# Performance work log

Measured on AMD Instinct MI355X. Metric: run time of the kernel, lower is better.

The kernel has to match this reference:

```python
import jax, jax.numpy as jnp
import numpy as np

N = 50000      # nodes
E = 800000     # edges (before self-loops)
DIN = 128
DH = 16        # per-head channels, layer 1
H = 8          # heads, layer 1
DOUT = 128     # layer 2 output (heads=1)
EDIM = 8       # edge_attr dim (unused by math: edge_dim=None in GATConv)
EPS_BN = 1e-5
NEG_SLOPE = 0.2


def _gat_conv(x, edge_index, W, a_src, a_dst, bias, heads, ch):
    """PyG GATConv (concat=True, add_self_loops=True, edge_dim=None)."""
    n = x.shape[0]
    loop = jnp.arange(n, dtype=edge_index.dtype)
    src = jnp.concatenate([edge_index[0], loop])  # [E+N]
    dst = jnp.concatenate([edge_index[1], loop])
    h = (x @ W).reshape(n, heads, ch)             # [N,H,C]
    s_src = jnp.einsum('nhc,hc->nh', h, a_src)    # [N,H]
    s_dst = jnp.einsum('nhc,hc->nh', h, a_dst)
    e = jax.nn.leaky_relu(s_src[src] + s_dst[dst], NEG_SLOPE)  # [E+N,H]
    # segment softmax over incoming edges of each dst node
    m = jax.ops.segment_max(e, dst, num_segments=n)
    ex = jnp.exp(e - m[dst])
    den = jax.ops.segment_sum(ex, dst, num_segments=n)
    alpha = ex / (den[dst] + 1e-16)               # [E+N,H]
    out = jax.ops.segment_sum(alpha[:, :, None] * h[src], dst, num_segments=n)
    return out.reshape(n, heads * ch) + bias


def _bn_selu(x, gamma, beta):
    # BatchNorm1d in training mode (batch statistics, biased variance) + SELU.
    mu = x.mean(axis=0)
    var = x.var(axis=0)
    xn = (x - mu) * jax.lax.rsqrt(var + EPS_BN)
    return jax.nn.selu(gamma * xn + beta)


def setup_inputs() -> dict:
    key = jax.random.key(0)
    ks = jax.random.split(key, 12)
    x = jax.random.normal(ks[0], (N, DIN), jnp.float32)
    edge_index = jax.random.randint(ks[1], (2, E), 0, N, jnp.int32)
    edge_attr = jax.random.normal(ks[2], (E, EDIM), jnp.float32)
    W1 = jax.random.normal(ks[3], (DIN, H * DH), jnp.float32) / np.sqrt(DIN)
    a_src1 = jax.random.normal(ks[4], (H, DH), jnp.float32) / np.sqrt(DH)
    a_dst1 = jax.random.normal(ks[5], (H, DH), jnp.float32) / np.sqrt(DH)
    b1 = jnp.zeros((H * DH,), jnp.float32)
    g1 = jnp.ones((H * DH,), jnp.float32)
    beta1 = jnp.zeros((H * DH,), jnp.float32)
    W2 = jax.random.normal(ks[6], (H * DH, DOUT), jnp.float32) / np.sqrt(H * DH)
    a_src2 = jax.random.normal(ks[7], (1, DOUT), jnp.float32) / np.sqrt(DOUT)
    a_dst2 = jax.random.normal(ks[8], (1, DOUT), jnp.float32) / np.sqrt(DOUT)
    b2 = jnp.zeros((DOUT,), jnp.float32)
    g2 = jnp.ones((DOUT,), jnp.float32)
    beta2 = jnp.zeros((DOUT,), jnp.float32)
    return dict(x=x, edge_index=edge_index, edge_attr=edge_attr,
                W1=W1, a_src1=a_src1, a_dst1=a_dst1, b1=b1, g1=g1, beta1=beta1,
                W2=W2, a_src2=a_src2, a_dst2=a_dst2, b2=b2, g2=g2, beta2=beta2)


def reference(x, edge_index, edge_attr,
              W1, a_src1, a_dst1, b1, g1, beta1,
              W2, a_src2, a_dst2, b2, g2, beta2):
    # edge_attr is unused: GATConv built with edge_dim=None ignores edge features.
    h = _gat_conv(x, edge_index, W1, a_src1, a_dst1, b1, H, DH)   # [N, H*DH]
    h = _bn_selu(h, g1, beta1)                                    # dropout = identity (eval)
    h = _gat_conv(h, edge_index, W2, a_src2, a_dst2, b2, 1, DOUT) # [N, DOUT]
    h = _bn_selu(h, g2, beta2)
    return h
```

## Files before the change

### kernel.cpp

```cpp
#include <hip/hip_runtime.h>

#define SELU_SCALE 1.0507009873554805f
#define SELU_ALPHA 1.6732632423543772f

typedef __attribute__((ext_vector_type(8))) short short8;
typedef __attribute__((ext_vector_type(4))) float f32x4;

#define BCAP 10240

static __device__ __forceinline__ float leaky02(float v) {
  return v > 0.0f ? v : 0.2f * v;
}

static __device__ __forceinline__ ushort f2bf(float f) {
  uint b = __float_as_uint(f);
  return (ushort)((b + 0x7fffu + ((b >> 16) & 1u)) >> 16);
}
static __device__ __forceinline__ float bf2f(ushort u) {
  return __uint_as_float(((uint)u) << 16);
}

static __device__ __forceinline__ float selu_f(float y) {
  return y > 0.f ? SELU_SCALE * y : SELU_SCALE * SELU_ALPHA * (__expf(y) - 1.f);
}

static __device__ __forceinline__ void load8(const float* p, float* xv, bool ok) {
  float4 xa = make_float4(0.f, 0.f, 0.f, 0.f), xb = xa;
  if (ok) {
    xa = *(const float4*)p;
    xb = *(const float4*)(p + 4);
  }
  xv[0] = xa.x; xv[1] = xa.y; xv[2] = xa.z; xv[3] = xa.w;
  xv[4] = xb.x; xv[5] = xb.y; xv[6] = xb.z; xv[7] = xb.w;
}
static __device__ __forceinline__ void load8(const ushort* p, float* xv, bool ok) {
  ushort4 ua = make_ushort4(0, 0, 0, 0), ub = ua;
  if (ok) {
    ua = *(const ushort4*)p;
    ub = *(const ushort4*)(p + 4);
  }
  xv[0] = bf2f(ua.x); xv[1] = bf2f(ua.y); xv[2] = bf2f(ua.z); xv[3] = bf2f(ua.w);
  xv[4] = bf2f(ub.x); xv[5] = bf2f(ub.y); xv[6] = bf2f(ub.z); xv[7] = bf2f(ub.w);
}

__global__ __launch_bounds__(256) void pack_kernel(const float* __restrict__ W1,
                                                   const float* __restrict__ W2,
                                                   ushort* __restrict__ Wp1,
                                                   ushort* __restrict__ Wp2,
                                                   float* __restrict__ zbase, int zwords) {
  if (blockIdx.x == 128) {
    for (int i = threadIdx.x; i < zwords; i += 256) zbase[i] = 0.f;
    return;
  }
  int idx = blockIdx.x * 256 + threadIdx.x;
  const float* W = (idx < 16384) ? W1 : W2;
  ushort* Wp = (idx < 16384) ? Wp1 : Wp2;
  int t = idx & 16383;
  int b = t & 7, i = (t >> 3) & 15, g = (t >> 7) & 3, kt = (t >> 9) & 3, ct = t >> 11;
  int k = kt * 32 + g * 8 + b, col = ct * 16 + i;
  Wp[t] = f2bf(W[k * 128 + col]);
}

template <int HEADS, bool BN, typename XT>
static __device__ __forceinline__ void gemm_body(
    int blk, const XT* __restrict__ X, const ushort* __restrict__ Wp,
    ushort* __restrict__ H, const float* __restrict__ asr, const float* __restrict__ adt,
    float* __restrict__ ssrc, float* __restrict__ sdst, int n,
    const float* __restrict__ stats, const float* __restrict__ gamma,
    const float* __restrict__ beta) {
  __shared__ float sc[128], sh[128];
  if (BN) {
    int t = threadIdx.x;
    if (t < 128) {
      float invN = 1.0f / (float)n;
      float mu = stats[t] * invN;
      float var = stats[128 + t] * invN - mu * mu;
      float rs = rsqrtf(var + 1e-5f);
      float s = gamma[t] * rs;
      sc[t] = s;
      sh[t] = beta[t] - s * mu;
    }
    __syncthreads();
  }
  const int tid = threadIdx.x;
  const int w = tid >> 6, l = tid & 63;
  const int lj = l & 15, lg = l >> 4;
  const int row = blk * 64 + w * 16 + lj;
  const bool rowok = row < n;
  const XT* xrow = X + (size_t)row * 128;

  f32x4 acc[8];
#pragma unroll
  for (int ct = 0; ct < 8; ++ct) acc[ct] = (f32x4){0.f, 0.f, 0.f, 0.f};

#pragma unroll
  for (int kt = 0; kt < 4; ++kt) {
    const int k0 = kt * 32 + lg * 8;
    float xv[8];
    load8(xrow + k0, xv, rowok);
    if (BN) {
#pragma unroll
      for (int b = 0; b < 8; ++b) xv[b] = selu_f(xv[b] * sc[k0 + b] + sh[k0 + b]);
    }
    short8 bx;
#pragma unroll
    for (int b = 0; b < 8; ++b) bx[b] = (short)f2bf(xv[b]);
#pragma unroll
    for (int ct = 0; ct < 8; ++ct) {
      short8 af = *(const short8*)(Wp + ((((ct * 4 + kt) * 4 + lg) * 16 + lj) << 3));
      acc[ct] = __builtin_amdgcn_mfma_f32_16x16x32_bf16(af, bx, acc[ct], 0, 0, 0);
    }
  }

  if (rowok) {
#pragma unroll
    for (int ct = 0; ct < 8; ++ct) {
      ushort4 h4;
      h4.x = f2bf(acc[ct][0]);
      h4.y = f2bf(acc[ct][1]);
      h4.z = f2bf(acc[ct][2]);
      h4.w = f2bf(acc[ct][3]);
      *(ushort4*)&H[(size_t)row * 128 + ct * 16 + lg * 4] = h4;
    }
  }

  if (HEADS == 8) {
    float ps[8], pd[8];
#pragma unroll
    for (int ct = 0; ct < 8; ++ct) {
      float4 av = *(const float4*)&asr[ct * 16 + lg * 4];
      float4 dv = *(const float4*)&adt[ct * 16 + lg * 4];
      ps[ct] = acc[ct][0] * av.x + acc[ct][1] * av.y + acc[ct][2] * av.z + acc[ct][3] * av.w;
      pd[ct] = acc[ct][0] * dv.x + acc[ct][1] * dv.y + acc[ct][2] * dv.z + acc[ct][3] * dv.w;
      ps[ct] += __shfl_xor(ps[ct], 16);
      ps[ct] += __shfl_xor(ps[ct], 32);
      pd[ct] += __shfl_xor(pd[ct], 16);
      pd[ct] += __shfl_xor(pd[ct], 32);
    }
    if (lg == 0 && rowok) {
      *(float4*)&ssrc[(size_t)row * 8] = make_float4(ps[0], ps[1], ps[2], ps[3]);
      *(float4*)&ssrc[(size_t)row * 8 + 4] = make_float4(ps[4], ps[5], ps[6], ps[7]);
      *(float4*)&sdst[(size_t)row * 8] = make_float4(pd[0], pd[1], pd[2], pd[3]);
      *(float4*)&sdst[(size_t)row * 8 + 4] = make_float4(pd[4], pd[5], pd[6], pd[7]);
    }
  } else {
    float ps = 0.f, pd = 0.f;
#pragma unroll
    for (int ct = 0; ct < 8; ++ct) {
      float4 av = *(const float4*)&asr[ct * 16 + lg * 4];
      float4 dv = *(const float4*)&adt[ct * 16 + lg * 4];
      ps += acc[ct][0] * av.x + acc[ct][1] * av.y + acc[ct][2] * av.z + acc[ct][3] * av.w;
      pd += acc[ct][0] * dv.x + acc[ct][1] * dv.y + acc[ct][2] * dv.z + acc[ct][3] * dv.w;
    }
    ps += __shfl_xor(ps, 16);
    ps += __shfl_xor(ps, 32);
    pd += __shfl_xor(pd, 16);
    pd += __shfl_xor(pd, 32);
    if (lg == 0 && rowok) {
      ssrc[row] = ps;
      sdst[row] = pd;
    }
  }
}

__global__ __launch_bounds__(256) void gemm1_bucket_kernel(
    const float* __restrict__ X, const ushort* __restrict__ Wp, ushort* __restrict__ H,
    const float* __restrict__ asr, const float* __restrict__ adt,
    float* __restrict__ ssrc, float* __restrict__ sdst, int n,
    const int* __restrict__ ei, int* __restrict__ gcur, uint* __restrict__ bucket,
    int nE, int EA, int NB, int gb) {
  if (blockIdx.x < gb) {
    gemm_body<8, false, float>(blockIdx.x, X, Wp, H, asr, adt, ssrc, sdst, n,
                               nullptr, nullptr, nullptr);
    return;
  }
  __shared__ int lcnt[128];
  __shared__ int lbase[128];
  int tid = threadIdx.x;
  if (tid < 128) lcnt[tid] = 0;
  __syncthreads();
  int e0 = (blockIdx.x - gb) * 1024;
  uint ent[4];
  int bk[4], lp[4];
#pragma unroll
  for (int j = 0; j < 4; ++j) {
    int e = e0 + j * 256 + tid;
    bk[j] = -1;
    if (e < EA) {
      int src, dst;
      if (e < nE) {
        src = ei[e];
        dst = ei[nE + e];
      } else {
        src = dst = e - nE;
      }
      bk[j] = dst >> 9;
      ent[j] = ((uint)src << 9) | (uint)(dst & 511);
      lp[j] = atomicAdd(&lcnt[bk[j]], 1);
    }
  }
  __syncthreads();
  if (tid < NB && lcnt[tid] > 0) lbase[tid] = atomicAdd(&gcur[tid], lcnt[tid]);
  __syncthreads();
#pragma unroll
  for (int j = 0; j < 4; ++j) {
    if (bk[j] >= 0) bucket[(size_t)bk[j] * BCAP + lbase[bk[j]] + lp[j]] = ent[j];
  }
}

__global__ __launch_bounds__(256) void gemm2_kernel(
    const ushort* __restrict__ X, const ushort* __restrict__ Wp, ushort* __restrict__ H,
    const float* __restrict__ asr, const float* __restrict__ adt,
    float* __restrict__ ssrc, float* __restrict__ sdst, int n,
    const float* __restrict__ stats, const float* __restrict__ gamma,
    const float* __restrict__ beta) {
  gemm_body<1, true, ushort>(blockIdx.x, X, Wp, H, asr, adt, ssrc, sdst, n,
                             stats, gamma, beta);
}

__global__ __launch_bounds__(1024) void csrbuild_kernel(const int* __restrict__ gcur,
                                                        const uint* __restrict__ bucket,
                                                        int* __restrict__ offs,
                                                        int* __restrict__ csr,
                                                        int n, int NB) {
  __shared__ int ldeg[512];
  __shared__ int loff[512];
  __shared__ int lwsum[8];
  __shared__ int partial[2];
  int b = blockIdx.x, tid = threadIdx.x;
  int lane = tid & 63, w = tid >> 6;
  if (tid < 128) {
    int v = (tid < b) ? gcur[tid] : 0;
#pragma unroll
    for (int s = 1; s < 64; s <<= 1) v += __shfl_xor(v, s);
    if (lane == 0) partial[tid >> 6] = v;
  }
  if (tid < 512) ldeg[tid] = 0;
  __syncthreads();
  int base = partial[0] + partial[1];
  int cnt = gcur[b];
  const uint* bb = bucket + (size_t)b * BCAP;
  for (int k = tid; k < cnt; k += 1024) atomicAdd(&ldeg[bb[k] & 511], 1);
  __syncthreads();
  int v = 0, x = 0;
  if (tid < 512) {
    v = ldeg[tid];
    x = v;
#pragma unroll
    for (int s = 1; s < 64; s <<= 1) {
      int t = __shfl_up(x, s);
      if (lane >= s) x += t;
    }
    if (lane == 63) lwsum[w] = x;
  }
  __syncthreads();
  if (w == 0 && lane < 8) {
    int wv = lwsum[lane];
    int y = wv;
#pragma unroll
    for (int s = 1; s < 8; s <<= 1) {
      int t = __shfl_up(y, s);
      if (lane >= s) y += t;
    }
    lwsum[lane] = y - wv;
  }
  __syncthreads();
  if (tid < 512) {
    int excl = x - v + lwsum[w];
    loff[tid] = excl;
    int node = b * 512 + tid;
    if (node < n) offs[node] = base + excl;
  }
  if (b == NB - 1 && tid == 0) offs[n] = base + cnt;
  __syncthreads();
  if (tid < 512) ldeg[tid] = loff[tid];
  __syncthreads();
  for (int k = tid; k < cnt; k += 1024) {
    uint e = bb[k];
    int pos = atomicAdd(&ldeg[e & 511], 1);
    csr[base + pos] = (int)(e >> 9);
  }
}

__global__ __launch_bounds__(256) void agg1_kernel(const ushort* __restrict__ h1,
                                                   const int* __restrict__ csr,
                                                   const int* __restrict__ offs,
                                                   const float* __restrict__ ssrc,
                                                   const float* __restrict__ sdst,
                                                   const float* __restrict__ bias,
                                                   ushort* __restrict__ outb, int nN) {
  int wid = (blockIdx.x * blockDim.x + threadIdx.x) >> 6;
  int lane = threadIdx.x & 63;
  int half = lane >> 5, ll = lane & 31;
  if (wid >= nN) return;
  int c = ll * 4;
  int h = ll >> 2;
  float sd = sdst[wid * 8 + h];
  int beg = offs[wid];
  int deg = offs[wid + 1] - beg;
  float a0 = 0.f, a1 = 0.f, a2 = 0.f, a3 = 0.f, den = 0.f;
  int i = half;
  for (; i + 6 < deg; i += 8) {
    int s0 = csr[beg + i];
    int s1 = csr[beg + i + 2];
    int s2 = csr[beg + i + 4];
    int s3 = csr[beg + i + 6];
    float e0 = ssrc[s0 * 8 + h];
    float e1 = ssrc[s1 * 8 + h];
    float e2 = ssrc[s2 * 8 + h];
    float e3 = ssrc[s3 * 8 + h];
    ushort4 u0 = *(const ushort4*)&h1[(size_t)s0 * 128 + c];
    ushort4 u1 = *(const ushort4*)&h1[(size_t)s1 * 128 + c];
    ushort4 u2 = *(const ushort4*)&h1[(size_t)s2 * 128 + c];
    ushort4 u3 = *(const ushort4*)&h1[(size_t)s3 * 128 + c];
    float A0 = __expf(leaky02(e0 + sd));
    float A1 = __expf(leaky02(e1 + sd));
    float A2 = __expf(leaky02(e2 + sd));
    float A3 = __expf(leaky02(e3 + sd));
    a0 += A0 * bf2f(u0.x) + A1 * bf2f(u1.x) + A2 * bf2f(u2.x) + A3 * bf2f(u3.x);
    a1 += A0 * bf2f(u0.y) + A1 * bf2f(u1.y) + A2 * bf2f(u2.y) + A3 * bf2f(u3.y);
    a2 += A0 * bf2f(u0.z) + A1 * bf2f(u1.z) + A2 * bf2f(u2.z) + A3 * bf2f(u3.z);
    a3 += A0 * bf2f(u0.w) + A1 * bf2f(u1.w) + A2 * bf2f(u2.w) + A3 * bf2f(u3.w);
    den += (A0 + A1) + (A2 + A3);
  }
  for (; i < deg; i += 2) {
    int s0 = csr[beg + i];
    float e0 = ssrc[s0 * 8 + h];
    ushort4 u0 = *(const ushort4*)&h1[(size_t)s0 * 128 + c];
    float A0 = __expf(leaky02(e0 + sd));
    a0 += A0 * bf2f(u0.x);
    a1 += A0 * bf2f(u0.y);
    a2 += A0 * bf2f(u0.z);
    a3 += A0 * bf2f(u0.w);
    den += A0;
  }
  a0 += __shfl_xor(a0, 32);
  a1 += __shfl_xor(a1, 32);
  a2 += __shfl_xor(a2, 32);
  a3 += __shfl_xor(a3, 32);
  den += __shfl_xor(den, 32);
  if (half == 0) {
    float invd = 1.0f / (den + 1e-16f);
    float4 bv = *(const float4*)&bias[c];
    ushort4 o;
    o.x = f2bf(a0 * invd + bv.x);
    o.y = f2bf(a1 * invd + bv.y);
    o.z = f2bf(a2 * invd + bv.z);
    o.w = f2bf(a3 * invd + bv.w);
    *(ushort4*)&outb[(size_t)wid * 128 + c] = o;
  }
}

__global__ __launch_bounds__(256) void agg2_kernel(const ushort* __restrict__ h2,
                                                   const int* __restrict__ csr,
                                                   const int* __restrict__ offs,
                                                   const float* __restrict__ ssrc,
                                                   const float* __restrict__ sdst,
                                                   const float* __restrict__ bias,
                                                   float* __restrict__ out, int nN) {
  int wid = (blockIdx.x * blockDim.x + threadIdx.x) >> 6;
  int lane = threadIdx.x & 63;
  int half = lane >> 5, ll = lane & 31;
  if (wid >= nN) return;
  int c = ll * 4;
  float sd = sdst[wid];
  int beg = offs[wid];
  int deg = offs[wid + 1] - beg;
  float a0 = 0.f, a1 = 0.f, a2 = 0.f, a3 = 0.f, den = 0.f;
  int i = half;
  for (; i + 6 < deg; i += 8) {
    int s0 = csr[beg + i];
    int s1 = csr[beg + i + 2];
    int s2 = csr[beg + i + 4];
    int s3 = csr[beg + i + 6];
    float e0 = ssrc[s0];
    float e1 = ssrc[s1];
    float e2 = ssrc[s2];
    float e3 = ssrc[s3];
    ushort4 u0 = *(const ushort4*)&h2[(size_t)s0 * 128 + c];
    ushort4 u1 = *(const ushort4*)&h2[(size_t)s1 * 128 + c];
    ushort4 u2 = *(const ushort4*)&h2[(size_t)s2 * 128 + c];
    ushort4 u3 = *(const ushort4*)&h2[(size_t)s3 * 128 + c];
    float A0 = __expf(leaky02(e0 + sd));
    float A1 = __expf(leaky02(e1 + sd));
    float A2 = __expf(leaky02(e2 + sd));
    float A3 = __expf(leaky02(e3 + sd));
    a0 += A0 * bf2f(u0.x) + A1 * bf2f(u1.x) + A2 * bf2f(u2.x) + A3 * bf2f(u3.x);
    a1 += A0 * bf2f(u0.y) + A1 * bf2f(u1.y) + A2 * bf2f(u2.y) + A3 * bf2f(u3.y);
    a2 += A0 * bf2f(u0.z) + A1 * bf2f(u1.z) + A2 * bf2f(u2.z) + A3 * bf2f(u3.z);
    a3 += A0 * bf2f(u0.w) + A1 * bf2f(u1.w) + A2 * bf2f(u2.w) + A3 * bf2f(u3.w);
    den += (A0 + A1) + (A2 + A3);
  }
  for (; i < deg; i += 2) {
    int s0 = csr[beg + i];
    float e0 = ssrc[s0];
    ushort4 u0 = *(const ushort4*)&h2[(size_t)s0 * 128 + c];
    float A0 = __expf(leaky02(e0 + sd));
    a0 += A0 * bf2f(u0.x);
    a1 += A0 * bf2f(u0.y);
    a2 += A0 * bf2f(u0.z);
    a3 += A0 * bf2f(u0.w);
    den += A0;
  }
  a0 += __shfl_xor(a0, 32);
  a1 += __shfl_xor(a1, 32);
  a2 += __shfl_xor(a2, 32);
  a3 += __shfl_xor(a3, 32);
  den += __shfl_xor(den, 32);
  if (half == 0) {
    float invd = 1.0f / (den + 1e-16f);
    float4 bv = *(const float4*)&bias[c];
    *(float4*)&out[(size_t)wid * 128 + c] =
        make_float4(a0 * invd + bv.x, a1 * invd + bv.y, a2 * invd + bv.z, a3 * invd + bv.w);
  }
}

__global__ __launch_bounds__(256) void stats_bf16_kernel(const ushort* __restrict__ X,
                                                         float* __restrict__ stats, int n) {
  __shared__ float red[256];
  int tid = threadIdx.x;
  int c = tid & 127;
  int half = tid >> 7;
  float s = 0.f, sq = 0.f;
  int rbeg = (int)blockIdx.x * 64 + half;
  int rend = min((int)(blockIdx.x + 1) * 64, n);
#pragma unroll 4
  for (int r = rbeg; r < rend; r += 2) {
    float v = bf2f(X[(size_t)r * 128 + c]);
    s += v;
    sq += v * v;
  }
  red[tid] = s;
  __syncthreads();
  float s2 = (half == 0) ? s + red[tid + 128] : 0.f;
  __syncthreads();
  red[tid] = sq;
  __syncthreads();
  if (half == 0) {
    float sq2 = sq + red[tid + 128];
    atomicAdd(&stats[c], s2);
    atomicAdd(&stats[128 + c], sq2);
  }
}

__global__ __launch_bounds__(256) void stats_kernel(const float* __restrict__ X,
                                                    float* __restrict__ stats, int n) {
  __shared__ float red[256];
  int tid = threadIdx.x;
  int c = tid & 127;
  int half = tid >> 7;
  float s = 0.f, sq = 0.f;
  int rbeg = (int)blockIdx.x * 64 + half;
  int rend = min((int)(blockIdx.x + 1) * 64, n);
#pragma unroll 4
  for (int r = rbeg; r < rend; r += 2) {
    float v = X[(size_t)r * 128 + c];
    s += v;
    sq += v * v;
  }
  red[tid] = s;
  __syncthreads();
  float s2 = (half == 0) ? s + red[tid + 128] : 0.f;
  __syncthreads();
  red[tid] = sq;
  __syncthreads();
  if (half == 0) {
    float sq2 = sq + red[tid + 128];
    atomicAdd(&stats[c], s2);
    atomicAdd(&stats[128 + c], sq2);
  }
}

__global__ __launch_bounds__(256) void bnselu_kernel(const float* __restrict__ X,
                                                     const float* __restrict__ stats,
                                                     const float* __restrict__ gamma,
                                                     const float* __restrict__ beta,
                                                     float* __restrict__ Y, int n) {
  int gid = blockIdx.x * blockDim.x + threadIdx.x;
  if (gid >= n * 32) return;
  int c = (gid & 31) * 4;
  int r = gid >> 5;
  float invN = 1.0f / (float)n;
  float4 x = *(const float4*)&X[(size_t)r * 128 + c];
  float o[4];
#pragma unroll
  for (int j = 0; j < 4; ++j) {
    float xx = (j == 0) ? x.x : (j == 1) ? x.y : (j == 2) ? x.z : x.w;
    float mu = stats[c + j] * invN;
    float var = stats[128 + c + j] * invN - mu * mu;
    float rs = rsqrtf(var + 1e-5f);
    float y = gamma[c + j] * ((xx - mu) * rs) + beta[c + j];
    o[j] = selu_f(y);
  }
  *(float4*)&Y[(size_t)r * 128 + c] = make_float4(o[0], o[1], o[2], o[3]);
}

extern "C" void kernel_launch(void* const* d_in, const int* in_sizes, int n_in,
                              void* d_out, int out_size, void* d_ws, size_t ws_size,
                              hipStream_t stream) {
  const float* x   = (const float*)d_in[0];
  const int*   ei  = (const int*)d_in[1];
  const float* W1  = (const float*)d_in[3];
  const float* as1 = (const float*)d_in[4];
  const float* ad1 = (const float*)d_in[5];
  const float* b1  = (const float*)d_in[6];
  const float* g1  = (const float*)d_in[7];
  const float* be1 = (const float*)d_in[8];
  const float* W2  = (const float*)d_in[9];
  const float* as2 = (const float*)d_in[10];
  const float* ad2 = (const float*)d_in[11];
  const float* b2  = (const float*)d_in[12];
  const float* g2  = (const float*)d_in[13];
  const float* be2 = (const float*)d_in[14];
  float* out = (float*)d_out;

  const int n  = in_sizes[0] / 128;
  const int nE = in_sizes[1] / 2;
  const int EA = nE + n;
  const int NB = (n + 511) >> 9;
  const int nbb = (EA + 1023) / 1024;
  const int gb = (n + 63) / 64;

  float* ws = (float*)d_ws;
  size_t o = 0;
  ushort* Bf = (ushort*)(ws + o); o += (size_t)n * 64;
  ushort* H = (ushort*)(ws + o); o += (size_t)n * 64;
  float* ssrc1 = ws + o;  o += (size_t)n * 8;
  float* sdst1 = ws + o;  o += (size_t)n * 8;
  float* ssrc2 = ws + o;  o += n;
  float* sdst2 = ws + o;  o += n;
  ushort* Wp1 = (ushort*)(ws + o); o += 8192;
  ushort* Wp2 = (ushort*)(ws + o); o += 8192;
  float* zbase = ws + o;
  float* stats1 = ws + o; o += 256;
  float* stats2 = ws + o; o += 256;
  int* gcur = (int*)(ws + o); o += 128;
  int zwords = (int)((ws + o) - zbase);
  int* offs = (int*)(ws + o); o += (size_t)n + 1;
  int* csr  = (int*)(ws + o); o += EA;
  uint* bucket = (uint*)(ws + o); o += (size_t)NB * BCAP;

  pack_kernel<<<129, 256, 0, stream>>>(W1, W2, Wp1, Wp2, zbase, zwords);

  gemm1_bucket_kernel<<<gb + nbb, 256, 0, stream>>>(
      x, Wp1, H, as1, ad1, ssrc1, sdst1, n, ei, gcur, bucket, nE, EA, NB, gb);
  csrbuild_kernel<<<NB, 1024, 0, stream>>>(gcur, bucket, offs, csr, n, NB);

  agg1_kernel<<<(n + 3) / 4, 256, 0, stream>>>(H, csr, offs, ssrc1, sdst1, b1, Bf, n);
  stats_bf16_kernel<<<(n + 63) / 64, 256, 0, stream>>>(Bf, stats1, n);

  gemm2_kernel<<<(n + 63) / 64, 256, 0, stream>>>(
      Bf, Wp2, H, as2, ad2, ssrc2, sdst2, n, stats1, g1, be1);
  agg2_kernel<<<(n + 3) / 4, 256, 0, stream>>>(H, csr, offs, ssrc2, sdst2, b2, out, n);
  stats_kernel<<<(n + 63) / 64, 256, 0, stream>>>(out, stats2, n);
  bnselu_kernel<<<(n * 32 + 255) / 256, 256, 0, stream>>>(out, stats2, g2, be2, out, n);
}
```

Measured before the change: 222.2 us.

## Fuse BatchNorm column statistics into aggregation kernels and widen per-lane gathers

The separate stats passes after each GAT aggregation are removed. Each aggregation block now accumulates per-column sum and sum-of-squares in shared memory via atomics, then flushes them to global stats. The lane mapping changes from 32 lanes × 4 channels with 2 edge streams to 16 lanes × 8 channels with 4 edge streams, using 16-byte bf16 gathers. This saves re-reading the output arrays and two launches, at the cost of shared and global atomics and an extra shuffle reduction stage.

```diff
diff --git a/kernel.cpp b/kernel.cpp
--- a/kernel.cpp
+++ b/kernel.cpp
@@ -288,66 +288,81 @@
                                                    const float* __restrict__ ssrc,
                                                    const float* __restrict__ sdst,
                                                    const float* __restrict__ bias,
-                                                   ushort* __restrict__ outb, int nN) {
-  int wid = (blockIdx.x * blockDim.x + threadIdx.x) >> 6;
-  int lane = threadIdx.x & 63;
-  int half = lane >> 5, ll = lane & 31;
-  if (wid >= nN) return;
-  int c = ll * 4;
-  int h = ll >> 2;
-  float sd = sdst[wid * 8 + h];
-  int beg = offs[wid];
-  int deg = offs[wid + 1] - beg;
-  float a0 = 0.f, a1 = 0.f, a2 = 0.f, a3 = 0.f, den = 0.f;
-  int i = half;
-  for (; i + 6 < deg; i += 8) {
+                                                   ushort* __restrict__ outb,
+                                                   float* __restrict__ stats, int nN) {
+  __shared__ float ssum[128], ssq[128];
+  int tid = threadIdx.x;
+  if (tid < 128) {
+    ssum[tid] = 0.f;
+    ssq[tid] = 0.f;
+  }
+  __syncthreads();
+  int wid = (blockIdx.x * 256 + tid) >> 6;
+  int lane = tid & 63;
+  int q = lane >> 4, ll = lane & 15;
+  bool ok = wid < nN;
+  int c = ll * 8;
+  int h = ll >> 1;
+  float sd = 0.f;
+  int beg = 0, deg = 0;
+  if (ok) {
+    sd = sdst[wid * 8 + h];
+    beg = offs[wid];
+    deg = offs[wid + 1] - beg;
+  }
+  float acc[8] = {0.f, 0.f, 0.f, 0.f, 0.f, 0.f, 0.f, 0.f};
+  float den = 0.f;
+  int i = q;
+  for (; i + 4 < deg; i += 8) {
     int s0 = csr[beg + i];
-    int s1 = csr[beg + i + 2];
-    int s2 = csr[beg + i + 4];
-    int s3 = csr[beg + i + 6];
+    int s1 = csr[beg + i + 4];
     float e0 = ssrc[s0 * 8 + h];
     float e1 = ssrc[s1 * 8 + h];
-    float e2 = ssrc[s2 * 8 + h];
-    float e3 = ssrc[s3 * 8 + h];
-    ushort4 u0 = *(const ushort4*)&h1[(size_t)s0 * 128 + c];
-    ushort4 u1 = *(const ushort4*)&h1[(size_t)s1 * 128 + c];
-    ushort4 u2 = *(const ushort4*)&h1[(size_t)s2 * 128 + c];
-    ushort4 u3 = *(const ushort4*)&h1[(size_t)s3 * 128 + c];
+    short8 u0 = *(const short8*)&h1[(size_t)s0 * 128 + c];
+    short8 u1 = *(const short8*)&h1[(size_t)s1 * 128 + c];
     float A0 = __expf(leaky02(e0 + sd));
     float A1 = __expf(leaky02(e1 + sd));
-    float A2 = __expf(leaky02(e2 + sd));
-    float A3 = __expf(leaky02(e3 + sd));
-    a0 += A0 * bf2f(u0.x) + A1 * bf2f(u1.x) + A2 * bf2f(u2.x) + A3 * bf2f(u3.x);
-    a1 += A0 * bf2f(u0.y) + A1 * bf2f(u1.y) + A2 * bf2f(u2.y) + A3 * bf2f(u3.y);
-    a2 += A0 * bf2f(u0.z) + A1 * bf2f(u1.z) + A2 * bf2f(u2.z) + A3 * bf2f(u3.z);
-    a3 += A0 * bf2f(u0.w) + A1 * bf2f(u1.w) + A2 * bf2f(u2.w) + A3 * bf2f(u3.w);
-    den += (A0 + A1) + (A2 + A3);
-  }
-  for (; i < deg; i += 2) {
+#pragma unroll
+    for (int j = 0; j < 8; ++j)
+      acc[j] += A0 * bf2f((ushort)u0[j]) + A1 * bf2f((ushort)u1[j]);
+    den += A0 + A1;
+  }
+  if (i < deg) {
     int s0 = csr[beg + i];
     float e0 = ssrc[s0 * 8 + h];
-    ushort4 u0 = *(const ushort4*)&h1[(size_t)s0 * 128 + c];
+    short8 u0 = *(const short8*)&h1[(size_t)s0 * 128 + c];
     float A0 = __expf(leaky02(e0 + sd));
-    a0 += A0 * bf2f(u0.x);
-    a1 += A0 * bf2f(u0.y);
-    a2 += A0 * bf2f(u0.z);
-    a3 += A0 * bf2f(u0.w);
+#pragma unroll
+    for (int j = 0; j < 8; ++j) acc[j] += A0 * bf2f((ushort)u0[j]);
     den += A0;
   }
-  a0 += __shfl_xor(a0, 32);
-  a1 += __shfl_xor(a1, 32);
-  a2 += __shfl_xor(a2, 32);
-  a3 += __shfl_xor(a3, 32);
+#pragma unroll
+  for (int j = 0; j < 8; ++j) {
+    acc[j] += __shfl_xor(acc[j], 16);
+    acc[j] += __shfl_xor(acc[j], 32);
+  }
+  den += __shfl_xor(den, 16);
   den += __shfl_xor(den, 32);
-  if (half == 0) {
+  if (q == 0 && ok) {
     float invd = 1.0f / (den + 1e-16f);
-    float4 bv = *(const float4*)&bias[c];
-    ushort4 o;
-    o.x = f2bf(a0 * invd + bv.x);
-    o.y = f2bf(a1 * invd + bv.y);
-    o.z = f2bf(a2 * invd + bv.z);
-    o.w = f2bf(a3 * invd + bv.w);
-    *(ushort4*)&outb[(size_t)wid * 128 + c] = o;
+    float4 bv0 = *(const float4*)&bias[c];
+    float4 bv1 = *(const float4*)&bias[c + 4];
+    float bb[8] = {bv0.x, bv0.y, bv0.z, bv0.w, bv1.x, bv1.y, bv1.z, bv1.w};
+    short8 o;
+#pragma unroll
+    for (int j = 0; j < 8; ++j) o[j] = (short)f2bf(acc[j] * invd + bb[j]);
+    *(short8*)&outb[(size_t)wid * 128 + c] = o;
+#pragma unroll
+    for (int j = 0; j < 8; ++j) {
+      float v = bf2f((ushort)o[j]);
+      atomicAdd(&ssum[c + j], v);
+      atomicAdd(&ssq[c + j], v * v);
+    }
+  }
+  __syncthreads();
+  if (tid < 128) {
+    atomicAdd(&stats[tid], ssum[tid]);
+    atomicAdd(&stats[128 + tid], ssq[tid]);
   }
 }
 
@@ -357,117 +372,80 @@
                                                    const float* __restrict__ ssrc,
                                                    const float* __restrict__ sdst,
                                                    const float* __restrict__ bias,
-                                                   float* __restrict__ out, int nN) {
-  int wid = (blockIdx.x * blockDim.x + threadIdx.x) >> 6;
-  int lane = threadIdx.x & 63;
-  int half = lane >> 5, ll = lane & 31;
-  if (wid >= nN) return;
-  int c = ll * 4;
-  float sd = sdst[wid];
-  int beg = offs[wid];
-  int deg = offs[wid + 1] - beg;
-  float a0 = 0.f, a1 = 0.f, a2 = 0.f, a3 = 0.f, den = 0.f;
-  int i = half;
-  for (; i + 6 < deg; i += 8) {
+                                                   float* __restrict__ out,
+                                                   float* __restrict__ stats, int nN) {
+  __shared__ float ssum[128], ssq[128];
+  int tid = threadIdx.x;
+  if (tid < 128) {
+    ssum[tid] = 0.f;
+    ssq[tid] = 0.f;
+  }
+  __syncthreads();
+  int wid = (blockIdx.x * 256 + tid) >> 6;
+  int lane = tid & 63;
+  int q = lane >> 4, ll = lane & 15;
+  bool ok = wid < nN;
+  int c = ll * 8;
+  float sd = 0.f;
+  int beg = 0, deg = 0;
+  if (ok) {
+    sd = sdst[wid];
+    beg = offs[wid];
+    deg = offs[wid + 1] - beg;
+  }
+  float acc[8] = {0.f, 0.f, 0.f, 0.f, 0.f, 0.f, 0.f, 0.f};
+  float den = 0.f;
+  int i = q;
+  for (; i + 4 < deg; i += 8) {
     int s0 = csr[beg + i];
-    int s1 = csr[beg + i + 2];
-    int s2 = csr[beg + i + 4];
-    int s3 = csr[beg + i + 6];
+    int s1 = csr[beg + i + 4];
     float e0 = ssrc[s0];
     float e1 = ssrc[s1];
-    float e2 = ssrc[s2];
-    float e3 = ssrc[s3];
-    ushort4 u0 = *(const ushort4*)&h2[(size_t)s0 * 128 + c];
-    ushort4 u1 = *(const ushort4*)&h2[(size_t)s1 * 128 + c];
-    ushort4 u2 = *(const ushort4*)&h2[(size_t)s2 * 128 + c];
-    ushort4 u3 = *(const ushort4*)&h2[(size_t)s3 * 128 + c];
+    short8 u0 = *(const short8*)&h2[(size_t)s0 * 128 + c];
+    short8 u1 = *(const short8*)&h2[(size_t)s1 * 128 + c];
     float A0 = __expf(leaky02(e0 + sd));
     float A1 = __expf(leaky02(e1 + sd));
-    float A2 = __expf(leaky02(e2 + sd));
-    float A3 = __expf(leaky02(e3 + sd));
-    a0 += A0 * bf2f(u0.x) + A1 * bf2f(u1.x) + A2 * bf2f(u2.x) + A3 * bf2f(u3.x);
-    a1 += A0 * bf2f(u0.y) + A1 * bf2f(u1.y) + A2 * bf2f(u2.y) + A3 * bf2f(u3.y);
-    a2 += A0 * bf2f(u0.z) + A1 * bf2f(u1.z) + A2 * bf2f(u2.z) + A3 * bf2f(u3.z);
-    a3 += A0 * bf2f(u0.w) + A1 * bf2f(u1.w) + A2 * bf2f(u2.w) + A3 * bf2f(u3.w);
-    den += (A0 + A1) + (A2 + A3);
-  }
-  for (; i < deg; i += 2) {
+#pragma unroll
+    for (int j = 0; j < 8; ++j)
+      acc[j] += A0 * bf2f((ushort)u0[j]) + A1 * bf2f((ushort)u1[j]);
+    den += A0 + A1;
+  }
+  if (i < deg) {
     int s0 = csr[beg + i];
     float e0 = ssrc[s0];
-    ushort4 u0 = *(const ushort4*)&h2[(size_t)s0 * 128 + c];
+    short8 u0 = *(const short8*)&h2[(size_t)s0 * 128 + c];
     float A0 = __expf(leaky02(e0 + sd));
-    a0 += A0 * bf2f(u0.x);
-    a1 += A0 * bf2f(u0.y);
-    a2 += A0 * bf2f(u0.z);
-    a3 += A0 * bf2f(u0.w);
+#pragma unroll
+    for (int j = 0; j < 8; ++j) acc[j] += A0 * bf2f((ushort)u0[j]);
     den += A0;
   }
-  a0 += __shfl_xor(a0, 32);
-  a1 += __shfl_xor(a1, 32);
-  a2 += __shfl_xor(a2, 32);
-  a3 += __shfl_xor(a3, 32);
+#pragma unroll
+  for (int j = 0; j < 8; ++j) {
+    acc[j] += __shfl_xor(acc[j], 16);
+    acc[j] += __shfl_xor(acc[j], 32);
+  }
+  den += __shfl_xor(den, 16);
   den += __shfl_xor(den, 32);
-  if (half == 0) {
+  if (q == 0 && ok) {
     float invd = 1.0f / (den + 1e-16f);
-    float4 bv = *(const float4*)&bias[c];
-    *(float4*)&out[(size_t)wid * 128 + c] =
-        make_float4(a0 * invd + bv.x, a1 * invd + bv.y, a2 * invd + bv.z, a3 * invd + bv.w);
-  }
-}
-
-__global__ __launch_bounds__(256) void stats_bf16_kernel(const ushort* __restrict__ X,
-                                                         float* __restrict__ stats, int n) {
-  __shared__ float red[256];
-  int tid = threadIdx.x;
-  int c = tid & 127;
-  int half = tid >> 7;
-  float s = 0.f, sq = 0.f;
-  int rbeg = (int)blockIdx.x * 64 + half;
-  int rend = min((int)(blockIdx.x + 1) * 64, n);
-#pragma unroll 4
-  for (int r = rbeg; r < rend; r += 2) {
-    float v = bf2f(X[(size_t)r * 128 + c]);
-    s += v;
-    sq += v * v;
-  }
-  red[tid] = s;
-  __syncthreads();
-  float s2 = (half == 0) ? s + red[tid + 128] : 0.f;
-  __syncthreads();
-  red[tid] = sq;
-  __syncthreads();
-  if (half == 0) {
-    float sq2 = sq + red[tid + 128];
-    atomicAdd(&stats[c], s2);
-    atomicAdd(&stats[128 + c], sq2);
-  }
-}
-
-__global__ __launch_bounds__(256) void stats_kernel(const float* __restrict__ X,
-                                                    float* __restrict__ stats, int n) {
-  __shared__ float red[256];
-  int tid = threadIdx.x;
-  int c = tid & 127;
-  int half = tid >> 7;
-  float s = 0.f, sq = 0.f;
-  int rbeg = (int)blockIdx.x * 64 + half;
-  int rend = min((int)(blockIdx.x + 1) * 64, n);
-#pragma unroll 4
-  for (int r = rbeg; r < rend; r += 2) {
-    float v = X[(size_t)r * 128 + c];
-    s += v;
-    sq += v * v;
-  }
-  red[tid] = s;
-  __syncthreads();
-  float s2 = (half == 0) ? s + red[tid + 128] : 0.f;
-  __syncthreads();
-  red[tid] = sq;
-  __syncthreads();
-  if (half == 0) {
-    float sq2 = sq + red[tid + 128];
-    atomicAdd(&stats[c], s2);
-    atomicAdd(&stats[128 + c], sq2);
+    float4 bv0 = *(const float4*)&bias[c];
+    float4 bv1 = *(const float4*)&bias[c + 4];
+    float bb[8] = {bv0.x, bv0.y, bv0.z, bv0.w, bv1.x, bv1.y, bv1.z, bv1.w};
+    float v[8];
+#pragma unroll
+    for (int j = 0; j < 8; ++j) v[j] = acc[j] * invd + bb[j];
+    *(float4*)&out[(size_t)wid * 128 + c] = make_float4(v[0], v[1], v[2], v[3]);
+    *(float4*)&out[(size_t)wid * 128 + c + 4] = make_float4(v[4], v[5], v[6], v[7]);
+#pragma unroll
+    for (int j = 0; j < 8; ++j) {
+      atomicAdd(&ssum[c + j], v[j]);
+      atomicAdd(&ssq[c + j], v[j] * v[j]);
+    }
+  }
+  __syncthreads();
+  if (tid < 128) {
+    atomicAdd(&stats[tid], ssum[tid]);
+    atomicAdd(&stats[128 + tid], ssq[tid]);
   }
 }
 
@@ -546,12 +524,12 @@
       x, Wp1, H, as1, ad1, ssrc1, sdst1, n, ei, gcur, bucket, nE, EA, NB, gb);
   csrbuild_kernel<<<NB, 1024, 0, stream>>>(gcur, bucket, offs, csr, n, NB);
 
-  agg1_kernel<<<(n + 3) / 4, 256, 0, stream>>>(H, csr, offs, ssrc1, sdst1, b1, Bf, n);
-  stats_bf16_kernel<<<(n + 63) / 64, 256, 0, stream>>>(Bf, stats1, n);
+  agg1_kernel<<<(n + 3) / 4, 256, 0, stream>>>(H, csr, offs, ssrc1, sdst1, b1, Bf,
+                                               stats1, n);
 
   gemm2_kernel<<<(n + 63) / 64, 256, 0, stream>>>(
       Bf, Wp2, H, as2, ad2, ssrc2, sdst2, n, stats1, g1, be1);
-  agg2_kernel<<<(n + 3) / 4, 256, 0, stream>>>(H, csr, offs, ssrc2, sdst2, b2, out, n);
-  stats_kernel<<<(n + 63) / 64, 256, 0, stream>>>(out, stats2, n);
+  agg2_kernel<<<(n + 3) / 4, 256, 0, stream>>>(H, csr, offs, ssrc2, sdst2, b2, out,
+                                               stats2, n);
   bnselu_kernel<<<(n * 32 + 255) / 256, 256, 0, stream>>>(out, stats2, g2, be2, out, n);
 }
```

Measured after the change: 727.4 us. +227.4%, slower.
